# Kernel optimization log

Measured on AMD Instinct MI355X. Metric: run time of the kernel, lower is better.

Reference implementation:

```python
import jax, jax.numpy as jnp
import numpy as np
from jax import lax

B, L, D, E, K, H = 8, 1024, 256, 8, 2, 1024  # batch, seq(in_channel), in_dim, experts, top_k, out_channel/hidden
LMAX = L // 2  # largest expert input dim (factor i+2 = 2)
LENS = [L // (i + 2) for i in range(E)]


def setup_inputs() -> dict:
    key = jax.random.key(0)
    ks = jax.random.split(key, 12)
    x = jax.random.normal(ks[0], (B, L, D), dtype=jnp.float32)
    conv_ws = jax.random.normal(ks[1], (3, D, D, 3), dtype=jnp.float32) / np.sqrt(3 * D)
    conv_bs = jax.random.normal(ks[2], (3, D), dtype=jnp.float32) * 0.01
    fl_w = jax.random.normal(ks[3], (E, L), dtype=jnp.float32) / np.sqrt(L)
    fl_b = jax.random.normal(ks[4], (E,), dtype=jnp.float32) * 0.01
    # expert first-layer weights, zero-padded on input axis to LMAX (expert i uses L//(i+2) inputs)
    w1 = jax.random.normal(ks[5], (E, H, LMAX), dtype=jnp.float32) / np.sqrt(LMAX)
    col_mask = (np.arange(LMAX)[None, :] < np.array(LENS)[:, None]).astype(np.float32)  # [E, LMAX]
    w1 = w1 * jnp.asarray(col_mask)[:, None, :]
    b1 = jax.random.normal(ks[6], (E, H), dtype=jnp.float32) * 0.01
    w2 = jax.random.normal(ks[7], (E, H, H), dtype=jnp.float32) / np.sqrt(H)
    b2 = jax.random.normal(ks[8], (E, H), dtype=jnp.float32) * 0.01
    w3 = jax.random.normal(ks[9], (E, H, H), dtype=jnp.float32) / np.sqrt(H)
    b3 = jax.random.normal(ks[10], (E, H), dtype=jnp.float32) * 0.01
    return {"x": x, "conv_ws": conv_ws, "conv_bs": conv_bs, "fl_w": fl_w, "fl_b": fl_b,
            "w1": w1, "b1": b1, "w2": w2, "b2": b2, "w3": w3, "b3": b3}


def _gelu(v):
    return jax.nn.gelu(v, approximate=False)  # torch nn.GELU default is exact erf


def _forward(x, conv_ws, conv_bs, fl_w, fl_b, w1, b1, w2, b2, w3, b3):
    xt = jnp.transpose(x, (0, 2, 1))  # [B, D, L]
    # --- Router: 3 dilated causal-padded ('same') convs + GELU ---
    h = xt
    for i in range(3):
        d = 2 ** i
        h = lax.conv_general_dilated(h, conv_ws[i], window_strides=(1,), padding=[(d, d)],
                                     rhs_dilation=(d,), dimension_numbers=("NCH", "OIH", "NCH"))
        h = _gelu(h + conv_bs[i][None, :, None])
    logits = jax.nn.sigmoid(jnp.einsum("bdl,el->bde", h, fl_w) + fl_b)  # [B, D, E]
    prob = jax.nn.softmax(logits, axis=-1)
    top_val, top_idx = lax.top_k(prob, K)  # [B, D, K]
    top_val = top_val / jnp.sum(top_val, axis=-1, keepdims=True)
    # combine gate per expert: gates[b,d,e] = sum_k top_val * 1[top_idx==e]
    gates = jnp.sum(top_val[..., None] * jax.nn.one_hot(top_idx, E, dtype=top_val.dtype), axis=2)  # [B, D, E]
    # --- Per-expert downsample (avg_pool1d, kernel=stride=i+2), zero-padded to LMAX ---
    xs = []
    for i in range(E):
        f = i + 2
        Li = LENS[i]
        xd = xt[:, :, :Li * f].reshape(B, D, Li, f).mean(-1)  # [B, D, Li]
        xs.append(jnp.pad(xd, ((0, 0), (0, 0), (0, LMAX - Li))))
    xe = jnp.stack(xs)  # [E, B, D, LMAX]; pad cols align with zeroed w1 cols
    # --- Expert MLPs (dense compute, masked by gates; zero gate == token not routed) ---
    h1 = _gelu(jnp.einsum("ebdl,ehl->ebdh", xe, w1) + b1[:, None, None, :])
    h2 = _gelu(jnp.einsum("ebdh,egh->ebdg", h1, w2) + b2[:, None, None, :])
    h3 = jnp.einsum("ebdg,eog->ebdo", h2, w3) + b3[:, None, None, :]  # [E, B, D, H]
    out = jnp.einsum("ebdo,bde->bdo", h3, gates)  # scatter-add combine, [B, D, H]
    return jnp.transpose(out, (0, 2, 1))  # [B, L(out_channel), D]


def reference(x, conv_ws, conv_bs, fl_w, fl_b, w1, b1, w2, b2, w3, b3):
    return _forward(x, conv_ws, conv_bs, fl_w, fl_b, w1, b1, w2, b2, w3, b3)
```

## Files before the change

kernel.cpp:

```cpp
#include <hip/hip_runtime.h>
#include <math.h>

#define Bb 8
#define Ll 1024
#define Dd 256
#define Ee 8
#define Hh 1024
#define LMAXc 512
#define NTOK (Bb*Dd)
#define LPAD 1032
#define MAXTILES 72

typedef short bf16x8 __attribute__((ext_vector_type(8)));
typedef float f32x4 __attribute__((ext_vector_type(4)));
typedef unsigned short u16x8 __attribute__((ext_vector_type(8)));

__device__ __forceinline__ float gelu_f(float x) {
    return 0.5f * x * (1.0f + erff(x * 0.70710678118654752440f));
}
__device__ __forceinline__ unsigned short f2b(float x) {
    unsigned int u = __float_as_uint(x);
    return (unsigned short)((u + 0x7fffu + ((u >> 16) & 1u)) >> 16);
}
__device__ __forceinline__ float b2f(unsigned short h) {
    return __uint_as_float(((unsigned int)h) << 16);
}
__device__ __forceinline__ void gl_lds16(const void* g, void* l) {
    __builtin_amdgcn_global_load_lds((const __attribute__((address_space(1))) unsigned int*)g,
                                     (__attribute__((address_space(3))) unsigned int*)l, 16, 0, 0);
}
__device__ __forceinline__ void split_one4(const float* __restrict__ src,
                                           unsigned short* __restrict__ hi,
                                           unsigned short* __restrict__ lo, int idx) {
    float4 v = ((const float4*)src)[idx];
    ushort2 h01, h23, l01, l23;
    unsigned short h;
    h = f2b(v.x); h01.x = h; l01.x = f2b(v.x - b2f(h));
    h = f2b(v.y); h01.y = h; l01.y = f2b(v.y - b2f(h));
    h = f2b(v.z); h23.x = h; l23.x = f2b(v.z - b2f(h));
    h = f2b(v.w); h23.y = h; l23.y = f2b(v.w - b2f(h));
    ((ushort2*)hi)[idx * 2] = h01; ((ushort2*)hi)[idx * 2 + 1] = h23;
    ((ushort2*)lo)[idx * 2] = l01; ((ushort2*)lo)[idx * 2 + 1] = l23;
}
__device__ __forceinline__ void cvt_one4(const float* __restrict__ src,
                                         unsigned short* __restrict__ dst, int idx) {
    float4 v = ((const float4*)src)[idx];
    ushort2 h01, h23;
    h01.x = f2b(v.x); h01.y = f2b(v.y);
    h23.x = f2b(v.z); h23.y = f2b(v.w);
    ((ushort2*)dst)[idx * 2] = h01; ((ushort2*)dst)[idx * 2 + 1] = h23;
}

__global__ __launch_bounds__(256) void prep_all(
    const float* __restrict__ x, const float* __restrict__ cw,
    const float* __restrict__ w1, const float* __restrict__ w2,
    const float* __restrict__ w3,
    unsigned short* __restrict__ xhi, unsigned short* __restrict__ xlo,
    unsigned short* __restrict__ chi, unsigned short* __restrict__ clo,
    unsigned short* __restrict__ wchi, unsigned short* __restrict__ wclo,
    unsigned short* __restrict__ w1hi, unsigned short* __restrict__ w1lo,
    unsigned short* __restrict__ w2b, unsigned short* __restrict__ w3b)
{
    int blk = blockIdx.x;
    int t = threadIdx.x;
    if (blk < 2048) {
        int idx = blk * 256 + t;
        int d4 = idx & 63;
        int l  = (idx >> 6) & 1023;
        int b  = idx >> 16;
        float4 v = ((const float4*)x)[idx];
        size_t o = ((size_t)(b * LPAD + 4 + l) * Dd + d4 * 4) >> 1;
        ushort2 h01, h23, l01, l23;
        unsigned short h;
        h = f2b(v.x); h01.x = h; l01.x = f2b(v.x - b2f(h));
        h = f2b(v.y); h01.y = h; l01.y = f2b(v.y - b2f(h));
        h = f2b(v.z); h23.x = h; l23.x = f2b(v.z - b2f(h));
        h = f2b(v.w); h23.y = h; l23.y = f2b(v.w - b2f(h));
        ((ushort2*)xhi)[o] = h01; ((ushort2*)xhi)[o + 1] = h23;
        ((ushort2*)xlo)[o] = l01; ((ushort2*)xlo)[o + 1] = l23;
    } else if (blk < 4352) {
        int idx = (blk - 2048) * 256 + t;
        int i = idx & (Dd - 1);
        int o = (idx >> 8) & (Dd - 1);
        int lk = idx >> 16;
        int layer = lk / 3;
        int k = lk % 3;
        float v = cw[(((size_t)layer * Dd + o) * Dd + i) * 3 + k];
        unsigned short h = f2b(v);
        wchi[idx] = h;
        wclo[idx] = f2b(v - b2f(h));
    } else if (blk < 8448) {
        split_one4(w1, w1hi, w1lo, (blk - 4352) * 256 + t);
    } else if (blk < 16640) {
        cvt_one4(w2, w2b, (blk - 8448) * 256 + t);
    } else if (blk < 24832) {
        cvt_one4(w3, w3b, (blk - 16640) * 256 + t);
    } else {
        int u = (blk - 24832) * 256 + t;
        int f = u >> 11;
        int rem = u & 2047;
        int b = rem >> 8;
        int r2 = rem & 255;
        int row = r2 >> 5;
        int col = (r2 & 31) * 8;
        int padrow = (row < 4) ? row : (1024 + row);
        unsigned short* buf = (f == 0) ? xhi : (f == 1) ? xlo : (f == 2) ? chi : clo;
        u16x8 z = {0, 0, 0, 0, 0, 0, 0, 0};
        *(u16x8*)(buf + (size_t)(b * LPAD + padrow) * Dd + col) = z;
    }
}

template<int MODE>
__global__ __launch_bounds__(256, 2) void conv_mfma(
    const unsigned short* __restrict__ inhi, const unsigned short* __restrict__ inlo,
    const unsigned short* __restrict__ whiL, const unsigned short* __restrict__ wloL,
    const float* __restrict__ bias,
    unsigned short* __restrict__ outhi, unsigned short* __restrict__ outlo,
    float* __restrict__ outf, int dil)
{
    __shared__ char smem[32768];
    char* sAhi = smem;
    char* sAlo = smem + 8192;
    char* sBhi = smem + 16384;
    char* sBlo = smem + 24576;

    const int t = threadIdx.x;
    const int lane = t & 63, w = t >> 6;
    const int r16 = lane & 15, quad = lane >> 4;
    const int wr = w >> 1, wc = w & 1;
    const int row0 = blockIdx.x * 64;
    const int col0 = blockIdx.y * 64;
    const int b = row0 >> 10, l0 = row0 & 1023;

    int aoff[2], boff[2];
    #pragma unroll
    for (int i = 0; i < 2; ++i) {
        int ra = wr * 32 + i * 16 + r16;
        aoff[i] = ra * 64 + ((quad ^ ((ra >> 1) & 3)) << 4);
        int rb = wc * 32 + i * 16 + r16;
        boff[i] = rb * 64 + ((quad ^ ((rb >> 1) & 3)) << 4);
    }
    const int rs = t >> 2, ce = ((t & 3) ^ ((rs >> 1) & 3)) << 3;
    const unsigned short* gAhi = inhi + (size_t)(b * LPAD + 4 + l0 + rs) * Dd + ce;
    const unsigned short* gAlo = inlo + (size_t)(b * LPAD + 4 + l0 + rs) * Dd + ce;

    f32x4 acc[2][2];
    const f32x4 zero4 = {0.f, 0.f, 0.f, 0.f};
    #pragma unroll
    for (int i = 0; i < 2; ++i)
        #pragma unroll
        for (int j = 0; j < 2; ++j) acc[i][j] = zero4;

    for (int tap = 0; tap < 3; ++tap) {
        const int sh = (tap - 1) * dil;
        const unsigned short* pAhi = gAhi + sh * Dd;
        const unsigned short* pAlo = gAlo + sh * Dd;
        const unsigned short* gBhi = whiL + ((size_t)tap * Dd + col0 + rs) * Dd + ce;
        const unsigned short* gBlo = wloL + ((size_t)tap * Dd + col0 + rs) * Dd + ce;
        for (int kb = 0; kb < Dd; kb += 64) {
            gl_lds16(pAhi + kb,      sAhi + (w << 10));
            gl_lds16(pAhi + kb + 32, sAhi + 4096 + (w << 10));
            gl_lds16(pAlo + kb,      sAlo + (w << 10));
            gl_lds16(pAlo + kb + 32, sAlo + 4096 + (w << 10));
            gl_lds16(gBhi + kb,      sBhi + (w << 10));
            gl_lds16(gBhi + kb + 32, sBhi + 4096 + (w << 10));
            gl_lds16(gBlo + kb,      sBlo + (w << 10));
            gl_lds16(gBlo + kb + 32, sBlo + 4096 + (w << 10));
            __syncthreads();
            #pragma unroll
            for (int h = 0; h < 2; ++h) {
                const int ho = h * 4096;
                bf16x8 ah[2], al[2], bh[2], bl[2];
                #pragma unroll
                for (int i = 0; i < 2; ++i) {
                    ah[i] = *(const bf16x8*)(sAhi + ho + aoff[i]);
                    al[i] = *(const bf16x8*)(sAlo + ho + aoff[i]);
                    bh[i] = *(const bf16x8*)(sBhi + ho + boff[i]);
                    bl[i] = *(const bf16x8*)(sBlo + ho + boff[i]);
                }
                #pragma unroll
                for (int mi = 0; mi < 2; ++mi)
                    #pragma unroll
                    for (int ni = 0; ni < 2; ++ni) {
                        acc[mi][ni] = __builtin_amdgcn_mfma_f32_16x16x32_bf16(ah[mi], bh[ni], acc[mi][ni], 0, 0, 0);
                        acc[mi][ni] = __builtin_amdgcn_mfma_f32_16x16x32_bf16(ah[mi], bl[ni], acc[mi][ni], 0, 0, 0);
                        acc[mi][ni] = __builtin_amdgcn_mfma_f32_16x16x32_bf16(al[mi], bh[ni], acc[mi][ni], 0, 0, 0);
                    }
            }
            __syncthreads();
        }
    }

    int cc[2]; float bv[2];
    #pragma unroll
    for (int ni = 0; ni < 2; ++ni) {
        cc[ni] = col0 + wc * 32 + ni * 16 + r16;
        bv[ni] = bias[cc[ni]];
    }
    #pragma unroll
    for (int mi = 0; mi < 2; ++mi) {
        int lb = l0 + wr * 32 + mi * 16 + quad * 4;
        #pragma unroll
        for (int reg = 0; reg < 4; ++reg) {
            int l = lb + reg;
            #pragma unroll
            for (int ni = 0; ni < 2; ++ni) {
                float v = gelu_f(acc[mi][ni][reg] + bv[ni]);
                if (MODE == 0) {
                    size_t o = (size_t)(b * LPAD + 4 + l) * Dd + cc[ni];
                    unsigned short h = f2b(v);
                    outhi[o] = h;
                    outlo[o] = f2b(v - b2f(h));
                } else {
                    outf[(size_t)(b * Ll + l) * Dd + cc[ni]] = v;
                }
            }
        }
    }
}

template<int MODE, int GATHER, int TWOPASS>
__global__ __launch_bounds__(256, 4) void gemm_sp(
    const unsigned short* __restrict__ AG,
    const unsigned short* __restrict__ BhiG, const unsigned short* __restrict__ BloG,
    const float* __restrict__ biasG, const float* __restrict__ gates,
    const int* __restrict__ cntG, const int* __restrict__ listG,
    const int* __restrict__ tileTab, const int* __restrict__ ntiles,
    unsigned short* __restrict__ Cout, float* __restrict__ outf,
    int M, int N, int K)
{
    if (blockIdx.y >= ntiles[0]) return;
    const int desc = tileTab[blockIdx.y];
    const int e = desc >> 16;
    const int row0 = (desc & 0xffff) * 64;
    const int cn = cntG[e];

    __shared__ char smem[TWOPASS ? 24576 : 16384];
    char* sA   = smem;
    char* sBhi = smem + 8192;
    char* sBlo = smem + 16384;

    const unsigned short* Bhi = BhiG + (size_t)e * N * K;
    const unsigned short* Blo = TWOPASS ? (BloG + (size_t)e * N * K) : nullptr;
    const float* bias = biasG + (size_t)e * N;

    const int t = threadIdx.x;
    const int lane = t & 63, w = t >> 6;
    const int r16 = lane & 15, quad = lane >> 4;
    const int wr = w >> 1, wc = w & 1;
    const int col0 = blockIdx.x * 64;

    int aoff[2], boff[2];
    #pragma unroll
    for (int i = 0; i < 2; ++i) {
        int ra = wr * 32 + i * 16 + r16;
        aoff[i] = ra * 64 + ((quad ^ ((ra >> 1) & 3)) << 4);
        int rb = wc * 32 + i * 16 + r16;
        boff[i] = rb * 64 + ((quad ^ ((rb >> 1) & 3)) << 4);
    }
    const int r0s = t >> 2, c0s = ((t & 3) ^ ((r0s >> 1) & 3)) << 3;
    int ri = row0 + r0s; if (ri > cn - 1) ri = cn - 1;
    const int ar = GATHER ? listG[e * NTOK + ri] : ri;
    const unsigned short* gA  = AG + ((size_t)e * M + ar) * K + c0s;
    const unsigned short* gB  = Bhi + (size_t)(col0 + r0s) * K + c0s;
    const unsigned short* gBl = TWOPASS ? (Blo + (size_t)(col0 + r0s) * K + c0s) : nullptr;
    const int wofs = w << 10;

    f32x4 acc[2][2];
    const f32x4 zero4 = {0.f, 0.f, 0.f, 0.f};
    #pragma unroll
    for (int i = 0; i < 2; ++i)
        #pragma unroll
        for (int j = 0; j < 2; ++j) acc[i][j] = zero4;

    for (int k0 = 0; k0 < K; k0 += 64) {
        gl_lds16(gA + k0,        sA + wofs);
        gl_lds16(gA + k0 + 32,   sA + 4096 + wofs);
        gl_lds16(gB + k0,        sBhi + wofs);
        gl_lds16(gB + k0 + 32,   sBhi + 4096 + wofs);
        if (TWOPASS) {
            gl_lds16(gBl + k0,      sBlo + wofs);
            gl_lds16(gBl + k0 + 32, sBlo + 4096 + wofs);
        }
        __syncthreads();
        #pragma unroll
        for (int h = 0; h < 2; ++h) {
            const int ho = h * 4096;
            bf16x8 ah[2], bh[2];
            #pragma unroll
            for (int i = 0; i < 2; ++i) {
                ah[i] = *(const bf16x8*)(sA + ho + aoff[i]);
                bh[i] = *(const bf16x8*)(sBhi + ho + boff[i]);
            }
            #pragma unroll
            for (int mi = 0; mi < 2; ++mi)
                #pragma unroll
                for (int ni = 0; ni < 2; ++ni)
                    acc[mi][ni] = __builtin_amdgcn_mfma_f32_16x16x32_bf16(ah[mi], bh[ni], acc[mi][ni], 0, 0, 0);
            if (TWOPASS) {
                bf16x8 bl[2];
                #pragma unroll
                for (int i = 0; i < 2; ++i) bl[i] = *(const bf16x8*)(sBlo + ho + boff[i]);
                #pragma unroll
                for (int mi = 0; mi < 2; ++mi)
                    #pragma unroll
                    for (int ni = 0; ni < 2; ++ni)
                        acc[mi][ni] = __builtin_amdgcn_mfma_f32_16x16x32_bf16(ah[mi], bl[ni], acc[mi][ni], 0, 0, 0);
            }
        }
        __syncthreads();
    }

    int cc[2]; float bv[2];
    #pragma unroll
    for (int ni = 0; ni < 2; ++ni) {
        cc[ni] = col0 + wc * 32 + ni * 16 + r16;
        bv[ni] = bias[cc[ni]];
    }
    if (MODE == 0) {
        unsigned short* CE = Cout + (size_t)e * M * N;
        #pragma unroll
        for (int mi = 0; mi < 2; ++mi) {
            int rb = row0 + wr * 32 + mi * 16 + quad * 4;
            #pragma unroll
            for (int reg = 0; reg < 4; ++reg) {
                size_t roff = (size_t)(rb + reg) * N;
                #pragma unroll
                for (int ni = 0; ni < 2; ++ni)
                    CE[roff + cc[ni]] = f2b(gelu_f(acc[mi][ni][reg] + bv[ni]));
            }
        }
    } else {
        #pragma unroll
        for (int mi = 0; mi < 2; ++mi) {
            int rb = row0 + wr * 32 + mi * 16 + quad * 4;
            #pragma unroll
            for (int reg = 0; reg < 4; ++reg) {
                int i = rb + reg;
                if (i < cn) {
                    int tok = listG[e * NTOK + i];
                    float g = gates[(size_t)tok * Ee + e];
                    size_t roff = (size_t)tok * N;
                    #pragma unroll
                    for (int ni = 0; ni < 2; ++ni)
                        atomicAdd(&outf[roff + cc[ni]], g * (acc[mi][ni][reg] + bv[ni]));
                }
            }
        }
    }
}


__global__ __launch_bounds__(256) void logits_accum(const float* __restrict__ h,
                                                    const float* __restrict__ fl_w,
                                                    float* __restrict__ logits) {
    int b = blockIdx.x;
    int chunk = blockIdx.y;
    __shared__ float wsm[Ee][128];
    for (int i = threadIdx.x; i < Ee * 128; i += 256) {
        int e = i >> 7, l = i & 127;
        wsm[e][l] = fl_w[e * Ll + chunk * 128 + l];
    }
    __syncthreads();
    int d = threadIdx.x;
    float acc[Ee] = {};
    for (int l = 0; l < 128; ++l) {
        float v = h[((size_t)b * Ll + chunk * 128 + l) * Dd + d];
        #pragma unroll
        for (int e = 0; e < Ee; ++e) acc[e] += v * wsm[e][l];
    }
    int tok = b * Dd + d;
    #pragma unroll
    for (int e = 0; e < Ee; ++e) atomicAdd(&logits[tok * Ee + e], acc[e]);
}

__global__ __launch_bounds__(1024) void gates_final(const float* __restrict__ logits,
                                                    const float* __restrict__ fl_b,
                                                    float* __restrict__ gates,
                                                    int* __restrict__ cnt,
                                                    int* __restrict__ list,
                                                    int* __restrict__ tileTab,
                                                    int* __restrict__ ntiles) {
    __shared__ int scnt[Ee];
    if (threadIdx.x < Ee) scnt[threadIdx.x] = 0;
    __syncthreads();
    const int lane = threadIdx.x & 63;
    const unsigned long long ltmask = (1ull << lane) - 1ull;

    for (int tok = threadIdx.x; tok < NTOK; tok += 1024) {
        float s[Ee];
        #pragma unroll
        for (int e = 0; e < Ee; ++e) {
            float z = logits[tok * Ee + e] + fl_b[e];
            s[e] = 1.0f / (1.0f + expf(-z));
        }
        float mx = s[0];
        #pragma unroll
        for (int e = 1; e < Ee; ++e) mx = fmaxf(mx, s[e]);
        float p[Ee];
        #pragma unroll
        for (int e = 0; e < Ee; ++e) p[e] = expf(s[e] - mx);
        int i1 = 0;
        #pragma unroll
        for (int e = 1; e < Ee; ++e) if (p[e] > p[i1]) i1 = e;
        int i2 = (i1 == 0) ? 1 : 0;
        #pragma unroll
        for (int e = 0; e < Ee; ++e) {
            if (e == i1 || e == i2) continue;
            if (p[e] > p[i2]) i2 = e;
        }
        float inv = 1.0f / (p[i1] + p[i2]);
        #pragma unroll
        for (int e = 0; e < Ee; ++e) gates[tok * Ee + e] = 0.0f;
        gates[tok * Ee + i1] = p[i1] * inv;
        gates[tok * Ee + i2] = p[i2] * inv;

        #pragma unroll
        for (int slot = 0; slot < 2; ++slot) {
            int ie = slot ? i2 : i1;
            for (int e = 0; e < Ee; ++e) {
                unsigned long long m = __ballot(ie == e);
                if (m) {
                    int leader = __ffsll((long long)m) - 1;
                    int base = 0;
                    if (lane == leader) base = atomicAdd(&scnt[e], (int)__popcll(m));
                    base = __shfl(base, leader);
                    if (ie == e) {
                        int pos = base + (int)__popcll(m & ltmask);
                        list[e * NTOK + pos] = tok;
                    }
                }
            }
        }
    }
    __syncthreads();
    if (threadIdx.x < Ee) cnt[threadIdx.x] = scnt[threadIdx.x];
    if (threadIdx.x == 0) {
        int nt = 0;
        for (int e = 0; e < Ee; ++e) {
            int c = scnt[e];
            for (int m = 0; m * 64 < c; ++m) tileTab[nt++] = (e << 16) | m;
        }
        ntiles[0] = nt;
    }
}

__global__ __launch_bounds__(256) void downsample_v3(const float* __restrict__ x,
                                                     unsigned short* __restrict__ xe) {
    int e = blockIdx.z;
    int f = e + 2;
    int Li = Ll / f;
    int j0 = blockIdx.x * 8;
    if (j0 >= Li) return;
    int b = blockIdx.y;
    int d = threadIdx.x;
    float invf = 1.0f / (float)f;
    int lim = Li - 1;
    float v[8] = {};
    for (int r = 0; r < f; ++r) {
        #pragma unroll
        for (int jj = 0; jj < 8; ++jj) {
            int j = j0 + jj; if (j > lim) j = lim;
            v[jj] += x[((size_t)(b * Ll + j * f + r)) * Dd + d];
        }
    }
    size_t obase = ((size_t)(e * NTOK + b * 256 + d)) * LMAXc + j0;
    if (j0 + 8 <= Li) {
        u16x8 hv;
        #pragma unroll
        for (int q = 0; q < 8; ++q) hv[q] = (short)f2b(v[q] * invf);
        *(u16x8*)(xe + obase) = hv;
    } else {
        for (int jj = 0; jj < Li - j0; ++jj)
            xe[obase + jj] = f2b(v[jj] * invf);
    }
}

__global__ __launch_bounds__(256) void transpose_out(const float* __restrict__ outacc,
                                                     float* __restrict__ out) {
    __shared__ float tile[32][33];
    int b = blockIdx.z;
    int d0 = blockIdx.x * 32;
    int o0 = blockIdx.y * 32;
    int tx = threadIdx.x & 31, ty = threadIdx.x >> 5;
    for (int i = 0; i < 32; i += 8)
        tile[ty + i][tx] = outacc[((size_t)b * Dd + d0 + ty + i) * Hh + o0 + tx];
    __syncthreads();
    for (int i = 0; i < 32; i += 8)
        out[((size_t)b * Hh + o0 + ty + i) * Dd + d0 + tx] = tile[tx][ty + i];
}

extern "C" void kernel_launch(void* const* d_in, const int* in_sizes, int n_in,
                              void* d_out, int out_size, void* d_ws, size_t ws_size,
                              hipStream_t stream) {
    const float* x       = (const float*)d_in[0];
    const float* conv_w  = (const float*)d_in[1];
    const float* conv_b  = (const float*)d_in[2];
    const float* fl_w    = (const float*)d_in[3];
    const float* fl_b    = (const float*)d_in[4];
    const float* w1      = (const float*)d_in[5];
    const float* b1      = (const float*)d_in[6];
    const float* w2      = (const float*)d_in[7];
    const float* b2      = (const float*)d_in[8];
    const float* w3      = (const float*)d_in[9];
    const float* b3      = (const float*)d_in[10];
    float* out = (float*)d_out;

    char* ws = (char*)d_ws;
    unsigned short* xphi = (unsigned short*)(ws);
    unsigned short* xplo = (unsigned short*)(ws + 4227072);
    unsigned short* cphi = (unsigned short*)(ws + 8454144);
    unsigned short* cplo = (unsigned short*)(ws + 12681216);
    unsigned short* wchi = (unsigned short*)(ws + 16908288);
    unsigned short* wclo = (unsigned short*)(ws + 18087936);
    float* hL            = (float*)(ws + 19267584);
    unsigned short* h1   = (unsigned short*)(ws);
    unsigned short* h2   = (unsigned short*)(ws + 33554432);
    unsigned short* xe   = (unsigned short*)(ws + 67108864);
    unsigned short* w1hi = (unsigned short*)(ws + 83886080);
    unsigned short* w1lo = (unsigned short*)(ws + 92274688);
    unsigned short* w2b  = (unsigned short*)(ws + 100663296);
    unsigned short* w3b  = (unsigned short*)(ws + 117440512);
    float* logits  = (float*)(ws + 134217728);
    int*   cnt     = (int*)(ws + 134283264);
    int*   ntiles  = (int*)(ws + 134283296);
    int*   tileTab = (int*)(ws + 134283328);
    float* gates   = (float*)(ws + 134284288);
    int*   list    = (int*)(ws + 134349824);
    float* outacc  = (float*)(ws);

    hipMemsetAsync(logits, 0, 65536 + 64, stream);

    prep_all<<<24864, 256, 0, stream>>>(x, conv_w, w1, w2, w3,
                                        xphi, xplo, cphi, cplo, wchi, wclo,
                                        w1hi, w1lo, w2b, w3b);

    const int WL = 3 * Dd * Dd;
    conv_mfma<0><<<dim3(Bb * Ll / 64, Dd / 64), 256, 0, stream>>>(
        xphi, xplo, wchi + 0 * WL, wclo + 0 * WL, conv_b + 0 * Dd, cphi, cplo, nullptr, 1);
    conv_mfma<0><<<dim3(Bb * Ll / 64, Dd / 64), 256, 0, stream>>>(
        cphi, cplo, wchi + 1 * WL, wclo + 1 * WL, conv_b + 1 * Dd, xphi, xplo, nullptr, 2);
    conv_mfma<1><<<dim3(Bb * Ll / 64, Dd / 64), 256, 0, stream>>>(
        xphi, xplo, wchi + 2 * WL, wclo + 2 * WL, conv_b + 2 * Dd, nullptr, nullptr, hL, 4);

    logits_accum<<<dim3(Bb, 8), 256, 0, stream>>>(hL, fl_w, logits);
    gates_final<<<1, 1024, 0, stream>>>(logits, fl_b, gates, cnt, list, tileTab, ntiles);

    downsample_v3<<<dim3(64, Bb, Ee), 256, 0, stream>>>(x, xe);

    gemm_sp<0, 1, 1><<<dim3(16, MAXTILES), 256, 0, stream>>>(
        xe, w1hi, w1lo, b1, nullptr, cnt, list, tileTab, ntiles, h1, nullptr, NTOK, Hh, LMAXc);

    gemm_sp<0, 0, 0><<<dim3(16, MAXTILES), 256, 0, stream>>>(
        h1, w2b, nullptr, b2, nullptr, cnt, list, tileTab, ntiles, h2, nullptr, NTOK, Hh, Hh);

    hipMemsetAsync(outacc, 0, (size_t)NTOK * Hh * sizeof(float), stream);

    gemm_sp<1, 0, 0><<<dim3(16, MAXTILES), 256, 0, stream>>>(
        h2, w3b, nullptr, b3, gates, cnt, list, tileTab, ntiles, nullptr, outacc, NTOK, Hh, Hh);

    transpose_out<<<dim3(Dd / 32, Hh / 32, Bb), 256, 0, stream>>>(outacc, out);
}
```

Before: 320.2 us.

## Fuse downsample into prep kernel, trim expert K range, deepen non-twopass K chunk

Moves the per-expert avg-pool downsample into the prep_all kernel as extra blocks, removing one launch. The first-layer gathered GEMM now stops its K loop at each expert's real input length rounded up to 64, skipping the all-zero padded columns. Single-pass GEMMs load four 32-wide K chunks per barrier instead of two, which halves the number of syncs but doubles shared memory to 32KB and may lower occupancy. The K trim assumes the xe columns past the rounded length are unused, and relies on those pad columns being zero in both xe and w1.

```diff
diff --git a/kernel.cpp b/kernel.cpp
--- a/kernel.cpp
+++ b/kernel.cpp
@@ -59,7 +59,8 @@
     unsigned short* __restrict__ chi, unsigned short* __restrict__ clo,
     unsigned short* __restrict__ wchi, unsigned short* __restrict__ wclo,
     unsigned short* __restrict__ w1hi, unsigned short* __restrict__ w1lo,
-    unsigned short* __restrict__ w2b, unsigned short* __restrict__ w3b)
+    unsigned short* __restrict__ w2b, unsigned short* __restrict__ w3b,
+    unsigned short* __restrict__ xe)
 {
     int blk = blockIdx.x;
     int t = threadIdx.x;
@@ -95,7 +96,7 @@
         cvt_one4(w2, w2b, (blk - 8448) * 256 + t);
     } else if (blk < 24832) {
         cvt_one4(w3, w3b, (blk - 16640) * 256 + t);
-    } else {
+    } else if (blk < 24864) {
         int u = (blk - 24832) * 256 + t;
         int f = u >> 11;
         int rem = u & 2047;
@@ -107,6 +108,36 @@
         unsigned short* buf = (f == 0) ? xhi : (f == 1) ? xlo : (f == 2) ? chi : clo;
         u16x8 z = {0, 0, 0, 0, 0, 0, 0, 0};
         *(u16x8*)(buf + (size_t)(b * LPAD + padrow) * Dd + col) = z;
+    } else {
+        int u = blk - 24864;
+        int e = u >> 9;
+        int b = (u >> 6) & 7;
+        int c = u & 63;
+        int f = e + 2;
+        int Li = Ll / f;
+        int j0 = c * 8;
+        if (j0 >= Li) return;
+        int d = t;
+        float invf = 1.0f / (float)f;
+        int lim = Li - 1;
+        float v[8] = {};
+        for (int r = 0; r < f; ++r) {
+            #pragma unroll
+            for (int jj = 0; jj < 8; ++jj) {
+                int j = j0 + jj; if (j > lim) j = lim;
+                v[jj] += x[((size_t)(b * Ll + j * f + r)) * Dd + d];
+            }
+        }
+        size_t obase = ((size_t)(e * NTOK + b * 256 + d)) * LMAXc + j0;
+        if (j0 + 8 <= Li) {
+            u16x8 hv;
+            #pragma unroll
+            for (int q = 0; q < 8; ++q) hv[q] = (short)f2b(v[q] * invf);
+            *(u16x8*)(xe + obase) = hv;
+        } else {
+            for (int jj = 0; jj < Li - j0; ++jj)
+                xe[obase + jj] = f2b(v[jj] * invf);
+        }
     }
 }
 
@@ -235,14 +266,21 @@
     const int row0 = (desc & 0xffff) * 64;
     const int cn = cntG[e];
 
-    __shared__ char smem[TWOPASS ? 24576 : 16384];
+    constexpr int NCH = TWOPASS ? 2 : 4;
+    __shared__ char smem[TWOPASS ? 24576 : 32768];
     char* sA   = smem;
-    char* sBhi = smem + 8192;
-    char* sBlo = smem + 16384;
+    char* sBhi = smem + NCH * 4096;
+    char* sBlo = smem + 2 * NCH * 4096;
 
     const unsigned short* Bhi = BhiG + (size_t)e * N * K;
     const unsigned short* Blo = TWOPASS ? (BloG + (size_t)e * N * K) : nullptr;
     const float* bias = biasG + (size_t)e * N;
+
+    int Keff = K;
+    if (GATHER) {
+        int Li = Ll / (e + 2);
+        Keff = ((Li + 63) >> 6) << 6;
+    }
 
     const int t = threadIdx.x;
     const int lane = t & 63, w = t >> 6;
@@ -273,18 +311,20 @@
         #pragma unroll
         for (int j = 0; j < 2; ++j) acc[i][j] = zero4;
 
-    for (int k0 = 0; k0 < K; k0 += 64) {
-        gl_lds16(gA + k0,        sA + wofs);
-        gl_lds16(gA + k0 + 32,   sA + 4096 + wofs);
-        gl_lds16(gB + k0,        sBhi + wofs);
-        gl_lds16(gB + k0 + 32,   sBhi + 4096 + wofs);
+    for (int k0 = 0; k0 < Keff; k0 += NCH * 32) {
+        #pragma unroll
+        for (int c = 0; c < NCH; ++c) {
+            gl_lds16(gA + k0 + c * 32, sA + c * 4096 + wofs);
+            gl_lds16(gB + k0 + c * 32, sBhi + c * 4096 + wofs);
+        }
         if (TWOPASS) {
-            gl_lds16(gBl + k0,      sBlo + wofs);
-            gl_lds16(gBl + k0 + 32, sBlo + 4096 + wofs);
+            #pragma unroll
+            for (int c = 0; c < NCH; ++c)
+                gl_lds16(gBl + k0 + c * 32, sBlo + c * 4096 + wofs);
         }
         __syncthreads();
         #pragma unroll
-        for (int h = 0; h < 2; ++h) {
+        for (int h = 0; h < NCH; ++h) {
             const int ho = h * 4096;
             bf16x8 ah[2], bh[2];
             #pragma unroll
@@ -442,37 +482,6 @@
             for (int m = 0; m * 64 < c; ++m) tileTab[nt++] = (e << 16) | m;
         }
         ntiles[0] = nt;
-    }
-}
-
-__global__ __launch_bounds__(256) void downsample_v3(const float* __restrict__ x,
-                                                     unsigned short* __restrict__ xe) {
-    int e = blockIdx.z;
-    int f = e + 2;
-    int Li = Ll / f;
-    int j0 = blockIdx.x * 8;
-    if (j0 >= Li) return;
-    int b = blockIdx.y;
-    int d = threadIdx.x;
-    float invf = 1.0f / (float)f;
-    int lim = Li - 1;
-    float v[8] = {};
-    for (int r = 0; r < f; ++r) {
-        #pragma unroll
-        for (int jj = 0; jj < 8; ++jj) {
-            int j = j0 + jj; if (j > lim) j = lim;
-            v[jj] += x[((size_t)(b * Ll + j * f + r)) * Dd + d];
-        }
-    }
-    size_t obase = ((size_t)(e * NTOK + b * 256 + d)) * LMAXc + j0;
-    if (j0 + 8 <= Li) {
-        u16x8 hv;
-        #pragma unroll
-        for (int q = 0; q < 8; ++q) hv[q] = (short)f2b(v[q] * invf);
-        *(u16x8*)(xe + obase) = hv;
-    } else {
-        for (int jj = 0; jj < Li - j0; ++jj)
-            xe[obase + jj] = f2b(v[jj] * invf);
     }
 }
 
@@ -531,9 +540,9 @@
 
     hipMemsetAsync(logits, 0, 65536 + 64, stream);
 
-    prep_all<<<24864, 256, 0, stream>>>(x, conv_w, w1, w2, w3,
+    prep_all<<<28960, 256, 0, stream>>>(x, conv_w, w1, w2, w3,
                                         xphi, xplo, cphi, cplo, wchi, wclo,
-                                        w1hi, w1lo, w2b, w3b);
+                                        w1hi, w1lo, w2b, w3b, xe);
 
     const int WL = 3 * Dd * Dd;
     conv_mfma<0><<<dim3(Bb * Ll / 64, Dd / 64), 256, 0, stream>>>(
@@ -546,8 +555,6 @@
     logits_accum<<<dim3(Bb, 8), 256, 0, stream>>>(hL, fl_w, logits);
     gates_final<<<1, 1024, 0, stream>>>(logits, fl_b, gates, cnt, list, tileTab, ntiles);
 
-    downsample_v3<<<dim3(64, Bb, Ee), 256, 0, stream>>>(x, xe);
-
     gemm_sp<0, 1, 1><<<dim3(16, MAXTILES), 256, 0, stream>>>(
         xe, w1hi, w1lo, b1, nullptr, cnt, list, tileTab, ntiles, h1, nullptr, NTOK, Hh, LMAXc);
 
```

Result: faster. 311.4 us (-2.8%).
